# Kernel tuning notes

Measured on AMD Instinct MI355X. Metric: run time of the kernel, lower is better.

## Reference

```python
import jax, jax.numpy as jnp
import numpy as np

N_NODES = 50000
N_EDGES = 1_600_000
N_REL = 8
D_IN = 128
D_OUT = 128


def _unique_edges(rng, n_nodes, n_rel, n_edges):
    # Torch module clamps the dense adjacency to 0/1, so duplicate
    # (rel, src, dst) triples collapse; generate unique edges so the
    # edge-list formulation matches exactly.
    m = 2 * n_edges
    src = rng.integers(0, n_nodes, m)
    dst = rng.integers(0, n_nodes, m)
    et = rng.integers(0, n_rel, m)
    key = (et.astype(np.int64) * n_nodes + src) * n_nodes + dst
    _, idx = np.unique(key, return_index=True)
    idx = np.sort(idx)[:n_edges]
    return src[idx], dst[idx], et[idx]


def setup_inputs() -> dict:
    key = jax.random.key(0)
    kx, kw, kr, kb = jax.random.split(key, 4)
    rng = np.random.default_rng(0)
    src, dst, et = _unique_edges(rng, N_NODES, N_REL, N_EDGES)
    bound = 1.0 / np.sqrt(D_OUT)
    return {
        "x": jax.random.normal(kx, (N_NODES, D_IN), dtype=jnp.float32),
        "edge_index": jnp.asarray(np.stack([src, dst]), dtype=jnp.int64),
        "edge_type": jnp.asarray(et, dtype=jnp.int64),
        "weight": jax.random.uniform(kw, (N_REL, D_OUT, D_IN), minval=-bound, maxval=bound, dtype=jnp.float32),
        "root": jax.random.uniform(kr, (D_OUT, D_IN), minval=-bound, maxval=bound, dtype=jnp.float32),
        "bias": jax.random.uniform(kb, (D_OUT,), minval=-bound, maxval=bound, dtype=jnp.float32),
    }


def reference(x, edge_index, edge_type, weight, root, bias):
    # Math identical to: adj[l, src, dst] = 1; adj row-normalized (mean);
    # out = sum_r norm_adj_r @ x @ W_r^T + x @ root^T + bias.
    n_rel, d_out, d_in = weight.shape
    n_nodes = x.shape[0]
    src = edge_index[0]
    dst = edge_index[1]
    seg = (edge_type * n_nodes + src).astype(jnp.int32)  # segment per (rel, node)
    num_seg = n_rel * n_nodes
    # sum of neighbor features per (relation, node): [R*N, d_in]
    agg = jax.ops.segment_sum(x[dst], seg, num_segments=num_seg)
    deg = jax.ops.segment_sum(jnp.ones((src.shape[0],), dtype=x.dtype), seg, num_segments=num_seg)
    norm = jnp.where(deg > 0, 1.0 / deg, 0.0)[:, None]  # mean aggr, nan_to_num(0)
    agg = (agg * norm).reshape(n_rel, n_nodes, d_in)
    out = jnp.einsum('rnd,rod->no', agg, weight)
    out = out + x @ root.T + bias[None]
    return out
```

## Files before the change

kernel.cpp:

```cpp
#include <hip/hip_runtime.h>


#define D 128
#define SCAN_CHUNK 2048
#define SEG_BITS 9
#define SEGS_PER_BUCKET 512
#define NBLK 128
#define APITCH 72

typedef __attribute__((ext_vector_type(8))) short short8;
typedef __attribute__((ext_vector_type(4))) float v4f;
typedef __attribute__((ext_vector_type(4))) unsigned uint4v;

__device__ __forceinline__ unsigned short f2b(float f) {
    union { float f; unsigned u; } v; v.f = f;
    unsigned r = v.u + 0x7fffu + ((v.u >> 16) & 1u);
    return (unsigned short)(r >> 16);
}
__device__ __forceinline__ float blo(unsigned u) {
    union { unsigned u; float f; } v; v.u = u << 16; return v.f;
}
__device__ __forceinline__ float bhi(unsigned u) {
    union { unsigned u; float f; } v; v.u = u & 0xffff0000u; return v.f;
}

__global__ void cvt_bf16_all(const float* __restrict__ x, long long nx,
                             const float* __restrict__ w, long long nw,
                             const float* __restrict__ root, long long nr,
                             unsigned short* __restrict__ xB,
                             unsigned short* __restrict__ wB) {
    long long i = ((long long)blockIdx.x * blockDim.x + threadIdx.x) * 4;
    const float* src;
    unsigned short* dst;
    long long j;
    if (i < nx) { src = x; dst = xB; j = i; }
    else if (i < nx + nw) { src = w; dst = wB; j = i - nx; }
    else if (i < nx + nw + nr) { src = root; dst = wB + nw; j = i - nx - nw; }
    else return;
    float4 v = *(const float4*)(src + j);
    uint2 p;
    p.x = (unsigned)f2b(v.x) | ((unsigned)f2b(v.y) << 16);
    p.y = (unsigned)f2b(v.z) | ((unsigned)f2b(v.w) << 16);
    *(uint2*)(dst + j) = p;
}

__global__ __launch_bounds__(256)
void histA(const int* __restrict__ ei, const int* __restrict__ et,
           int* __restrict__ blockHist, int nE, int nN, int B, int epb) {
    __shared__ int lh[1024];
    const int tid = threadIdx.x;
    for (int b = tid; b < B; b += 256) lh[b] = 0;
    __syncthreads();
    const int base = blockIdx.x * epb;
    const int lim = min(base + epb, nE);
    for (int e = base + tid; e < lim; e += 256) {
        int seg = et[e] * nN + ei[e];
        atomicAdd(&lh[seg >> SEG_BITS], 1);
    }
    __syncthreads();
    for (int b = tid; b < B; b += 256)
        blockHist[b * NBLK + blockIdx.x] = lh[b];
}

__global__ __launch_bounds__(256)
void scan1(const int* __restrict__ in, int* __restrict__ excl,
           int* __restrict__ blockSums, int n) {
    __shared__ int t[256];
    const int tid = threadIdx.x;
    const int base = blockIdx.x * SCAN_CHUNK + tid * 8;
    int v[8];
    int tot = 0;
#pragma unroll
    for (int i = 0; i < 8; i++) {
        v[i] = (base + i < n) ? in[base + i] : 0;
        tot += v[i];
    }
    t[tid] = tot;
    __syncthreads();
    for (int off = 1; off < 256; off <<= 1) {
        int add = (tid >= off) ? t[tid - off] : 0;
        __syncthreads();
        t[tid] += add;
        __syncthreads();
    }
    int run = t[tid] - tot;
#pragma unroll
    for (int i = 0; i < 8; i++) {
        if (base + i < n) excl[base + i] = run;
        run += v[i];
    }
    if (tid == 255) blockSums[blockIdx.x] = t[255];
}

__global__ __launch_bounds__(256)
void scan2(int* __restrict__ blockSums, int nb) {
    __shared__ int t[256];
    const int tid = threadIdx.x;
    int v = (tid < nb) ? blockSums[tid] : 0;
    t[tid] = v;
    __syncthreads();
    for (int off = 1; off < 256; off <<= 1) {
        int add = (tid >= off) ? t[tid - off] : 0;
        __syncthreads();
        t[tid] += add;
        __syncthreads();
    }
    if (tid < nb) blockSums[tid] = t[tid] - v;
}

__global__ __launch_bounds__(256)
void scan3s(int* __restrict__ excl, const int* __restrict__ blockSums, int n) {
    const int base = blockIdx.x * SCAN_CHUNK + threadIdx.x * 8;
    const int bs = blockSums[blockIdx.x];
#pragma unroll
    for (int i = 0; i < 8; i++)
        if (base + i < n) excl[base + i] += bs;
}

__global__ __launch_bounds__(256)
void scatterA(const int* __restrict__ ei, const int* __restrict__ et,
              const int* __restrict__ scanned, unsigned* __restrict__ bucketEdges,
              int nE, int nN, int B, int epb) {
    __shared__ int cur[1024];
    const int tid = threadIdx.x;
    for (int b = tid; b < B; b += 256) cur[b] = scanned[b * NBLK + blockIdx.x];
    __syncthreads();
    const int base = blockIdx.x * epb;
    const int lim = min(base + epb, nE);
    for (int e = base + tid; e < lim; e += 256) {
        int seg = et[e] * nN + ei[e];
        int bkt = seg >> SEG_BITS;
        unsigned pk = ((unsigned)(seg & (SEGS_PER_BUCKET - 1)) << 16) | (unsigned)ei[nE + e];
        int pos = atomicAdd(&cur[bkt], 1);
        bucketEdges[pos] = pk;
    }
}

__global__ __launch_bounds__(256)
void segOff(const unsigned* __restrict__ bucketEdges, const int* __restrict__ scanned,
            int* __restrict__ off, unsigned short* __restrict__ sortedDst,
            int nE, int numSeg, int B) {
    __shared__ int lh[SEGS_PER_BUCKET];
    __shared__ int sc[256];
    __shared__ int lcur[SEGS_PER_BUCKET];
    const int tid = threadIdx.x;
    const int b = blockIdx.x;
    const int eBase = scanned[b * NBLK];
    const int eEnd = (b + 1 < B) ? scanned[(b + 1) * NBLK] : nE;
    const int segBase = b * SEGS_PER_BUCKET;
    const int segLim = min(SEGS_PER_BUCKET, numSeg - segBase);

    lh[2 * tid] = 0; lh[2 * tid + 1] = 0;
    __syncthreads();
    for (int i = eBase + tid; i < eEnd; i += 256)
        atomicAdd(&lh[bucketEdges[i] >> 16], 1);
    __syncthreads();
    int a0 = lh[2 * tid], a1 = lh[2 * tid + 1];
    sc[tid] = a0 + a1;
    __syncthreads();
    for (int o = 1; o < 256; o <<= 1) {
        int add = (tid >= o) ? sc[tid - o] : 0;
        __syncthreads();
        sc[tid] += add;
        __syncthreads();
    }
    int pairBase = sc[tid] - (a0 + a1);
    int g0 = eBase + pairBase;
    int g1 = g0 + a0;
    lcur[2 * tid] = g0;
    lcur[2 * tid + 1] = g1;
    if (2 * tid < segLim)     off[segBase + 2 * tid] = g0;
    if (2 * tid + 1 < segLim) off[segBase + 2 * tid + 1] = g1;
    if (b == B - 1 && tid == 0) off[numSeg] = nE;
    __syncthreads();
    for (int i = eBase + tid; i < eEnd; i += 256) {
        unsigned u = bucketEdges[i];
        int pos = atomicAdd(&lcur[u >> 16], 1);
        sortedDst[pos] = (unsigned short)(u & 0xFFFFu);
    }
}

__global__ __launch_bounds__(256)
void rgcn_gather(const unsigned short* __restrict__ xB,
                 const unsigned short* __restrict__ sortedDst,
                 const int* __restrict__ off,
                 unsigned short* __restrict__ aggB, int nN) {
    const int tid = threadIdx.x;
    const int lane = tid & 63;
    const int idx16 = lane & 15;
    const int grp = lane >> 4;
    const int wv = tid >> 6;
    const int n = blockIdx.x * 16 + wv * 4 + grp;
    const int r = blockIdx.y;
    const bool valid = (n < nN);
    const int seg = valid ? (r * nN + n) : 0;

    const int start = off[seg];
    int cnt = valid ? (off[seg + 1] - start) : 0;

    int mx = cnt;
    mx = max(mx, __shfl_xor(mx, 16));
    mx = max(mx, __shfl_xor(mx, 32));

    float2 acc2[4];
#pragma unroll
    for (int i = 0; i < 4; i++) acc2[i] = make_float2(0.f, 0.f);

    const unsigned short* xChunk = xB + idx16 * 8;

    for (int b = 0; b < mx; b += 16) {
        int myDst = (b + idx16 < cnt) ? (int)sortedDst[start + b + idx16] : 0;
        int kcap = min(16, mx - b);
        for (int g = 0; g < kcap; g += 4) {
            uint4v v[4];
#pragma unroll
            for (int j = 0; j < 4; j++) {
                int k = g + j;
                int dst = __shfl(myDst, grp * 16 + k);
                bool act = (k < kcap) && (b + k < cnt);
                v[j] = act ? *(const uint4v*)(xChunk + ((size_t)dst << 7))
                           : (uint4v){0u, 0u, 0u, 0u};
            }
#pragma unroll
            for (int j = 0; j < 4; j++) {
                acc2[0].x += blo(v[j].x); acc2[0].y += bhi(v[j].x);
                acc2[1].x += blo(v[j].y); acc2[1].y += bhi(v[j].y);
                acc2[2].x += blo(v[j].z); acc2[2].y += bhi(v[j].z);
                acc2[3].x += blo(v[j].w); acc2[3].y += bhi(v[j].w);
            }
        }
    }

    if (valid) {
        float s = cnt > 0 ? 1.0f / (float)cnt : 0.f;
        uint4v pkt;
        pkt.x = (unsigned)f2b(acc2[0].x * s) | ((unsigned)f2b(acc2[0].y * s) << 16);
        pkt.y = (unsigned)f2b(acc2[1].x * s) | ((unsigned)f2b(acc2[1].y * s) << 16);
        pkt.z = (unsigned)f2b(acc2[2].x * s) | ((unsigned)f2b(acc2[2].y * s) << 16);
        pkt.w = (unsigned)f2b(acc2[3].x * s) | ((unsigned)f2b(acc2[3].y * s) << 16);
        __builtin_nontemporal_store(pkt, (uint4v*)(aggB + (size_t)seg * D + idx16 * 8));
    }
}

__global__ __launch_bounds__(256)
void rgcn_gemm_mfma(const unsigned short* __restrict__ aggB,
                    const unsigned short* __restrict__ xB,
                    const unsigned short* __restrict__ wB,
                    const float* __restrict__ bias,
                    float* __restrict__ out, int nN, int nRel) {
    __shared__ __align__(16) unsigned short As[64 * APITCH];
    __shared__ __align__(16) unsigned short Bs[128 * APITCH];
    const int tid = threadIdx.x;
    const int wave = tid >> 6;
    const int lane = tid & 63;
    const int wm = wave & 1;
    const int wn = wave >> 1;
    const int m16 = lane & 15;
    const int q = lane >> 4;
    const int row0 = blockIdx.x * 64;

    v4f acc[2][4];
#pragma unroll
    for (int i = 0; i < 2; i++)
#pragma unroll
        for (int j = 0; j < 4; j++) acc[i][j] = (v4f){0.f, 0.f, 0.f, 0.f};

    const int nSlabs = nRel + 1;
    for (int s = 0; s < nSlabs; s++) {
        const unsigned short* aSrc = (s < nRel) ? (aggB + (size_t)s * nN * D) : xB;
        const unsigned short* bSrc = wB + (size_t)s * D * D;
        for (int h = 0; h < 2; h++) {
            const int dbase = h * 64;
#pragma unroll
            for (int p = 0; p < 2; p++) {
                int idx = tid + p * 256;
                int arow = idx >> 3;
                int ch = idx & 7;
                int n = row0 + arow;
                uint4 v = make_uint4(0u, 0u, 0u, 0u);
                if (n < nN)
                    v = *(const uint4*)(aSrc + (size_t)n * D + dbase + ch * 8);
                *(uint4*)&As[arow * APITCH + ch * 8] = v;
            }
#pragma unroll
            for (int p = 0; p < 4; p++) {
                int idx = tid + p * 256;
                int o = idx >> 3;
                int ch = idx & 7;
                uint4 v = *(const uint4*)(bSrc + (size_t)o * D + dbase + ch * 8);
                *(uint4*)&Bs[o * APITCH + ch * 8] = v;
            }
            __syncthreads();

#pragma unroll
            for (int kb = 0; kb < 64; kb += 32) {
                short8 a[2], b[4];
#pragma unroll
                for (int mt = 0; mt < 2; mt++)
                    a[mt] = *(const short8*)&As[(wm * 32 + mt * 16 + m16) * APITCH + kb + q * 8];
#pragma unroll
                for (int nt = 0; nt < 4; nt++)
                    b[nt] = *(const short8*)&Bs[(wn * 64 + nt * 16 + m16) * APITCH + kb + q * 8];
#pragma unroll
                for (int mt = 0; mt < 2; mt++)
#pragma unroll
                    for (int nt = 0; nt < 4; nt++)
                        acc[mt][nt] = __builtin_amdgcn_mfma_f32_16x16x32_bf16(
                            a[mt], b[nt], acc[mt][nt], 0, 0, 0);
            }
            __syncthreads();
        }
    }

#pragma unroll
    for (int mt = 0; mt < 2; mt++) {
#pragma unroll
        for (int nt = 0; nt < 4; nt++) {
            int col = wn * 64 + nt * 16 + m16;
            float bi = bias[col];
#pragma unroll
            for (int reg = 0; reg < 4; reg++) {
                int rrow = row0 + wm * 32 + mt * 16 + q * 4 + reg;
                if (rrow < nN)
                    out[(size_t)rrow * D + col] = acc[mt][nt][reg] + bi;
            }
        }
    }
}

extern "C" void kernel_launch(void* const* d_in, const int* in_sizes, int n_in,
                              void* d_out, int out_size, void* d_ws, size_t ws_size,
                              hipStream_t stream) {
    const float* x    = (const float*)d_in[0];
    const int*   ei   = (const int*)d_in[1];
    const int*   et   = (const int*)d_in[2];
    const float* w    = (const float*)d_in[3];
    const float* root = (const float*)d_in[4];
    const float* bias = (const float*)d_in[5];
    float* out = (float*)d_out;

    const int nN   = in_sizes[0] / D;
    const int nE   = in_sizes[2];
    const int nRel = in_sizes[3] / (D * D);
    const int numSeg = nRel * nN;
    const int B = (numSeg + SEGS_PER_BUCKET - 1) >> SEG_BITS;
    const int nBH = B * NBLK;
    const int epb = (nE + NBLK - 1) / NBLK;

    char* p = (char*)d_ws;
    unsigned* bucketEdges   = (unsigned*)p;        p += (size_t)nE * sizeof(unsigned);
    unsigned short* sortedDst = (unsigned short*)p; p += (size_t)nE * sizeof(unsigned short);
    p = (char*)(((uintptr_t)p + 255) & ~(uintptr_t)255);
    int* off       = (int*)p;  p += (size_t)(numSeg + 1) * sizeof(int);
    int* blockHist = (int*)p;  p += (size_t)nBH * sizeof(int);
    int* scanned   = (int*)p;  p += (size_t)nBH * sizeof(int);
    int* blockSums = (int*)p;  p += 256 * sizeof(int);
    p = (char*)(((uintptr_t)p + 255) & ~(uintptr_t)255);
    unsigned short* xB   = (unsigned short*)p;  p += (size_t)nN * D * sizeof(unsigned short);
    unsigned short* wB   = (unsigned short*)p;  p += (size_t)(nRel + 1) * D * D * sizeof(unsigned short);
    p = (char*)(((uintptr_t)p + 255) & ~(uintptr_t)255);
    unsigned short* aggB = (unsigned short*)p;

    const int nScanBlocks = (nBH + SCAN_CHUNK - 1) / SCAN_CHUNK;

    histA<<<NBLK, 256, 0, stream>>>(ei, et, blockHist, nE, nN, B, epb);
    scan1<<<nScanBlocks, 256, 0, stream>>>(blockHist, scanned, blockSums, nBH);
    scan2<<<1, 256, 0, stream>>>(blockSums, nScanBlocks);
    scan3s<<<nScanBlocks, 256, 0, stream>>>(scanned, blockSums, nBH);
    scatterA<<<NBLK, 256, 0, stream>>>(ei, et, scanned, bucketEdges, nE, nN, B, epb);
    segOff<<<B, 256, 0, stream>>>(bucketEdges, scanned, off, sortedDst, nE, numSeg, B);

    long long nx = (long long)nN * D;
    long long nw = (long long)nRel * D * D;
    long long nr = (long long)D * D;
    long long ncvt = (nx + nw + nr) / 4;
    cvt_bf16_all<<<(int)((ncvt + 255) / 256), 256, 0, stream>>>(x, nx, w, nw, root, nr, xB, wB);

    dim3 gg((nN + 15) / 16, nRel);
    rgcn_gather<<<gg, 256, 0, stream>>>(xB, sortedDst, off, aggB, nN);

    rgcn_gemm_mfma<<<(nN + 63) / 64, 256, 0, stream>>>(aggB, xB, wB, bias, out, nN, nRel);
}
```

Measured before the change: 280.7 us.

## Split bf16 x into four 32-column slabs to shrink gather working set

The bf16 copy of x is stored as four column slabs of 32 features each ([4][N][32]). The gather kernel adds a grid z-dimension over slabs, so each launch slice touches only a quarter-width table (about 3.2 MB), which can stay resident in L2/MALL while edges are gathered. Each node is now handled by 4 lanes instead of 16, and the GEMM's x-slab loads are updated for the new layout. In exchange, the edge index lists are read four times, each gather load is a 64-byte row fragment, and the loop is bounded by the maximum degree across 16 nodes per wave, which can cause more divergence.

```diff
diff --git a/kernel.cpp b/kernel.cpp
--- a/kernel.cpp
+++ b/kernel.cpp
@@ -28,13 +28,23 @@
                              const float* __restrict__ w, long long nw,
                              const float* __restrict__ root, long long nr,
                              unsigned short* __restrict__ xB,
-                             unsigned short* __restrict__ wB) {
+                             unsigned short* __restrict__ wB, int nN) {
     long long i = ((long long)blockIdx.x * blockDim.x + threadIdx.x) * 4;
+    if (i < nx) {
+        float4 v = *(const float4*)(x + i);
+        uint2 p;
+        p.x = (unsigned)f2b(v.x) | ((unsigned)f2b(v.y) << 16);
+        p.y = (unsigned)f2b(v.z) | ((unsigned)f2b(v.w) << 16);
+        long long n = i >> 7;
+        int d = (int)(i & 127);
+        size_t o = (size_t)(d >> 5) * (size_t)nN * 32 + (size_t)n * 32 + (d & 31);
+        *(uint2*)(xB + o) = p;
+        return;
+    }
     const float* src;
     unsigned short* dst;
     long long j;
-    if (i < nx) { src = x; dst = xB; j = i; }
-    else if (i < nx + nw) { src = w; dst = wB; j = i - nx; }
+    if (i < nx + nw) { src = w; dst = wB; j = i - nx; }
     else if (i < nx + nw + nr) { src = root; dst = wB + nw; j = i - nx - nw; }
     else return;
     float4 v = *(const float4*)(src + j);
@@ -187,11 +197,12 @@
                  unsigned short* __restrict__ aggB, int nN) {
     const int tid = threadIdx.x;
     const int lane = tid & 63;
-    const int idx16 = lane & 15;
-    const int grp = lane >> 4;
+    const int idx4 = lane & 3;
+    const int grp = lane >> 2;
     const int wv = tid >> 6;
-    const int n = blockIdx.x * 16 + wv * 4 + grp;
+    const int n = blockIdx.x * 64 + wv * 16 + grp;
     const int r = blockIdx.y;
+    const int sl = blockIdx.z;
     const bool valid = (n < nN);
     const int seg = valid ? (r * nN + n) : 0;
 
@@ -199,6 +210,8 @@
     int cnt = valid ? (off[seg + 1] - start) : 0;
 
     int mx = cnt;
+    mx = max(mx, __shfl_xor(mx, 4));
+    mx = max(mx, __shfl_xor(mx, 8));
     mx = max(mx, __shfl_xor(mx, 16));
     mx = max(mx, __shfl_xor(mx, 32));
 
@@ -206,28 +219,24 @@
 #pragma unroll
     for (int i = 0; i < 4; i++) acc2[i] = make_float2(0.f, 0.f);
 
-    const unsigned short* xChunk = xB + idx16 * 8;
-
-    for (int b = 0; b < mx; b += 16) {
-        int myDst = (b + idx16 < cnt) ? (int)sortedDst[start + b + idx16] : 0;
-        int kcap = min(16, mx - b);
-        for (int g = 0; g < kcap; g += 4) {
-            uint4v v[4];
-#pragma unroll
-            for (int j = 0; j < 4; j++) {
-                int k = g + j;
-                int dst = __shfl(myDst, grp * 16 + k);
-                bool act = (k < kcap) && (b + k < cnt);
-                v[j] = act ? *(const uint4v*)(xChunk + ((size_t)dst << 7))
-                           : (uint4v){0u, 0u, 0u, 0u};
-            }
-#pragma unroll
-            for (int j = 0; j < 4; j++) {
-                acc2[0].x += blo(v[j].x); acc2[0].y += bhi(v[j].x);
-                acc2[1].x += blo(v[j].y); acc2[1].y += bhi(v[j].y);
-                acc2[2].x += blo(v[j].z); acc2[2].y += bhi(v[j].z);
-                acc2[3].x += blo(v[j].w); acc2[3].y += bhi(v[j].w);
-            }
+    const unsigned short* xSlab = xB + (size_t)sl * nN * 32 + idx4 * 8;
+
+    for (int b = 0; b < mx; b += 4) {
+        int myDst = (b + idx4 < cnt) ? (int)sortedDst[start + b + idx4] : 0;
+        uint4v v[4];
+#pragma unroll
+        for (int j = 0; j < 4; j++) {
+            int dst = __shfl(myDst, grp * 4 + j);
+            bool act = (b + j < cnt);
+            v[j] = act ? *(const uint4v*)(xSlab + ((size_t)dst << 5))
+                       : (uint4v){0u, 0u, 0u, 0u};
+        }
+#pragma unroll
+        for (int j = 0; j < 4; j++) {
+            acc2[0].x += blo(v[j].x); acc2[0].y += bhi(v[j].x);
+            acc2[1].x += blo(v[j].y); acc2[1].y += bhi(v[j].y);
+            acc2[2].x += blo(v[j].z); acc2[2].y += bhi(v[j].z);
+            acc2[3].x += blo(v[j].w); acc2[3].y += bhi(v[j].w);
         }
     }
 
@@ -238,7 +247,7 @@
         pkt.y = (unsigned)f2b(acc2[1].x * s) | ((unsigned)f2b(acc2[1].y * s) << 16);
         pkt.z = (unsigned)f2b(acc2[2].x * s) | ((unsigned)f2b(acc2[2].y * s) << 16);
         pkt.w = (unsigned)f2b(acc2[3].x * s) | ((unsigned)f2b(acc2[3].y * s) << 16);
-        __builtin_nontemporal_store(pkt, (uint4v*)(aggB + (size_t)seg * D + idx16 * 8));
+        __builtin_nontemporal_store(pkt, (uint4v*)(aggB + (size_t)seg * D + sl * 32 + idx4 * 8));
     }
 }
 
@@ -267,7 +276,8 @@
 
     const int nSlabs = nRel + 1;
     for (int s = 0; s < nSlabs; s++) {
-        const unsigned short* aSrc = (s < nRel) ? (aggB + (size_t)s * nN * D) : xB;
+        const bool isX = (s == nRel);
+        const unsigned short* aSrc = isX ? xB : (aggB + (size_t)s * nN * D);
         const unsigned short* bSrc = wB + (size_t)s * D * D;
         for (int h = 0; h < 2; h++) {
             const int dbase = h * 64;
@@ -278,8 +288,14 @@
                 int ch = idx & 7;
                 int n = row0 + arow;
                 uint4 v = make_uint4(0u, 0u, 0u, 0u);
-                if (n < nN)
-                    v = *(const uint4*)(aSrc + (size_t)n * D + dbase + ch * 8);
+                if (n < nN) {
+                    if (isX) {
+                        int c8 = dbase + ch * 8;
+                        v = *(const uint4*)(aSrc + ((size_t)(c8 >> 5) * nN + n) * 32 + (c8 & 31));
+                    } else {
+                        v = *(const uint4*)(aSrc + (size_t)n * D + dbase + ch * 8);
+                    }
+                }
                 *(uint4*)&As[arow * APITCH + ch * 8] = v;
             }
 #pragma unroll
@@ -374,9 +390,9 @@
     long long nw = (long long)nRel * D * D;
     long long nr = (long long)D * D;
     long long ncvt = (nx + nw + nr) / 4;
-    cvt_bf16_all<<<(int)((ncvt + 255) / 256), 256, 0, stream>>>(x, nx, w, nw, root, nr, xB, wB);
-
-    dim3 gg((nN + 15) / 16, nRel);
+    cvt_bf16_all<<<(int)((ncvt + 255) / 256), 256, 0, stream>>>(x, nx, w, nw, root, nr, xB, wB, nN);
+
+    dim3 gg((nN + 63) / 64, nRel, 4);
     rgcn_gather<<<gg, 256, 0, stream>>>(xB, sortedDst, off, aggB, nN);
 
     rgcn_gemm_mfma<<<(nN + 63) / 64, 256, 0, stream>>>(aggB, xB, wB, bias, out, nN, nRel);
```

Measured after the change: 295.5 us. 1.05x slower.
